# Kernel optimization log

Measured on AMD Instinct MI355X. Metric: run time of the kernel, lower is better.

Reference implementation:

```python
import jax, jax.numpy as jnp
import numpy as np
import math

L, D, H, PK, N = 3, 512, 8, 8, 3072
DK = D // H


def _layernorm(x, s, b):
    m = jnp.mean(x, axis=-1, keepdims=True)
    v = jnp.mean((x - m) ** 2, axis=-1, keepdims=True)
    return (x - m) / jnp.sqrt(v + 1e-6) * s + b


def setup_inputs() -> dict:
    key = jax.random.key(0)
    ks = jax.random.split(key, 12)
    p = lambda k, shape: jax.random.normal(k, shape, jnp.float32) * (1.0 / math.sqrt(shape[-1]))
    x = jax.random.normal(ks[0], (N, D), jnp.float32)
    adm = jax.random.randint(ks[1], (N, N), 0, PK, jnp.int32)
    return {
        "x": x,
        "adm": adm,
        "ln_att_s": jnp.ones((L, D), jnp.float32),
        "ln_att_b": jnp.zeros((L, D), jnp.float32),
        "Wq": p(ks[2], (L, D, D)),
        "Wk": p(ks[3], (L, D, D)),
        "Wv": p(ks[4], (L, D, D)),
        "rel_k": p(ks[5], (L, PK, DK)),
        "Wg": p(ks[6], (L, D, D)) * 0.0,  # gating weight init to 0 in original
        "bg": jnp.ones((L, D), jnp.float32),  # gating bias init to 1
        "Wo": p(ks[7], (L, D, D)),
        "bo": jnp.zeros((L, D), jnp.float32),
        "ln_ff_s": jnp.ones((L, D), jnp.float32),
        "ln_ff_b": jnp.zeros((L, D), jnp.float32),
        "W1": p(ks[8], (L, D, 2 * D)),
        "b1": jnp.zeros((L, 2 * D), jnp.float32),
        "W2": p(ks[9], (L, 2 * D, D)),
        "b2": jnp.zeros((L, D), jnp.float32),
    }


def reference(x, adm, ln_att_s, ln_att_b, Wq, Wk, Wv, rel_k, Wg, bg, Wo, bo,
              ln_ff_s, ln_ff_b, W1, b1, W2, b2):
    att_scores = []
    idx = jnp.broadcast_to(adm[None], (H, N, N))  # one_hot(gpm) @ r  ==  gather r along PK
    for n in range(L):
        xn = _layernorm(x, ln_att_s[n], ln_att_b[n])  # same layer_norm applied to x_q and x_k
        q = (xn @ Wq[n]).reshape(N, H, DK).transpose(1, 0, 2)  # [H,N,DK]
        k = (xn @ Wk[n]).reshape(N, H, DK).transpose(1, 0, 2)
        v = (xn @ Wv[n]).reshape(N, H, DK).transpose(1, 0, 2)
        attn1 = jnp.einsum('hid,hjd->hij', q, k)  # [H,N,N]
        rq = jnp.einsum('hid,pd->hip', q, rel_k[n])  # [H,N,PK]
        attn2 = jnp.take_along_axis(rq, idx, axis=2)  # [H,N,N]
        attn = jax.nn.softmax((attn1 + attn2) / math.sqrt(DK), axis=-1)
        out = jnp.einsum('hij,hjd->hid', attn, v).transpose(1, 0, 2).reshape(N, D)
        gate = jax.nn.sigmoid(xn @ Wg[n] + bg[n])
        m = (out * gate) @ Wo[n] + bo[n]
        # FFN with pre-layernorm, residual: x = x + pff(x + m)
        y = x + m
        yn = _layernorm(y, ln_ff_s[n], ln_ff_b[n])
        ff = jax.nn.gelu(yn @ W1[n] + b1[n], approximate=True) @ W2[n] + b2[n]
        x = x + ff
        att_scores.append(attn)
    return (x, jnp.stack(att_scores))
```

## Files before the change

kernel.cpp:

```cpp
#include <hip/hip_runtime.h>
#include <math.h>

#define NT 3072
#define DIM 512
#define NH 8
#define DKH 64
#define PKN 8
#define D2 1024
#define NL 3
#define QS 2048

typedef float4 f4;
typedef unsigned short ushort_t;
typedef unsigned char uchar_t;
typedef __attribute__((ext_vector_type(8))) short s8x;
typedef __attribute__((ext_vector_type(4))) float fx4;

#define MFMA(a, b, c) __builtin_amdgcn_mfma_f32_16x16x32_bf16(a, b, c, 0, 0, 0)
#define EX2(x) __builtin_amdgcn_exp2f(x)

__device__ __forceinline__ float b2f(ushort_t u) {
  union { unsigned int x; float f; } c;
  c.x = (unsigned int)u << 16;
  return c.f;
}
__device__ __forceinline__ ushort_t f2b(float f) {
  union { float f; unsigned int x; } c;
  c.f = f;
  unsigned int r = (c.x + 0x7FFFu + ((c.x >> 16) & 1u)) >> 16;
  return (ushort_t)r;
}
__device__ __forceinline__ float wred_sum(float v) {
#pragma unroll
  for (int off = 32; off > 0; off >>= 1) v += __shfl_xor(v, off);
  return v;
}
__device__ __forceinline__ void gload16(const ushort_t* g, ushort_t* l) {
  __builtin_amdgcn_global_load_lds(
      (const __attribute__((address_space(1))) unsigned int*)(const void*)g,
      (__attribute__((address_space(3))) unsigned int*)(void*)l, 16, 0, 0);
}

__global__ __launch_bounds__(256) void ln_bf16_kernel(
    const float* __restrict__ x, const float* __restrict__ s,
    const float* __restrict__ b, ushort_t* __restrict__ out) {
  int row = blockIdx.x;
  const float* xr = x + (size_t)row * DIM;
  int t = threadIdx.x;
  float v0 = xr[t], v1 = xr[t + 256];
  float sum = wred_sum(v0 + v1);
  float sq = wred_sum(v0 * v0 + v1 * v1);
  __shared__ float ss[4], s2[4];
  if ((t & 63) == 0) { ss[t >> 6] = sum; s2[t >> 6] = sq; }
  __syncthreads();
  float tot = ss[0] + ss[1] + ss[2] + ss[3];
  float tot2 = s2[0] + s2[1] + s2[2] + s2[3];
  float mean = tot * (1.0f / DIM);
  float var = tot2 * (1.0f / DIM) - mean * mean;
  float inv = rsqrtf(var + 1e-6f);
  ushort_t* orow = out + (size_t)row * DIM;
  orow[t] = f2b((v0 - mean) * inv * s[t] + b[t]);
  orow[t + 256] = f2b((v1 - mean) * inv * s[t + 256] + b[t + 256]);
}

__device__ __forceinline__ void tconv_body(const float* __restrict__ W,
                                           ushort_t* __restrict__ Wt, int K,
                                           int Nc, int tx, int ty) {
  __shared__ float Ls[64][65];
  int t = threadIdx.x;
  int n0 = tx * 64, k0 = ty * 64;
  int rr = t >> 4, cc = (t & 15) * 4;
#pragma unroll
  for (int p = 0; p < 4; ++p) {
    f4 v = *(const f4*)&W[(size_t)(k0 + rr + p * 16) * Nc + n0 + cc];
    Ls[rr + p * 16][cc + 0] = v.x;
    Ls[rr + p * 16][cc + 1] = v.y;
    Ls[rr + p * 16][cc + 2] = v.z;
    Ls[rr + p * 16][cc + 3] = v.w;
  }
  __syncthreads();
  int nr = t >> 2, kc = (t & 3) * 16;
  ushort_t tmp[16];
#pragma unroll
  for (int e = 0; e < 16; ++e) tmp[e] = f2b(Ls[kc + e][nr]);
  ushort_t* dst = &Wt[(size_t)(n0 + nr) * K + k0 + kc];
  *(uint4*)dst = *(uint4*)&tmp[0];
  *(uint4*)(dst + 8) = *(uint4*)&tmp[8];
}

__global__ __launch_bounds__(256) void wprep_kernel(
    const float* __restrict__ Wq, const float* __restrict__ Wk,
    const float* __restrict__ Wv, const float* __restrict__ Wg,
    const float* __restrict__ Wo, const float* __restrict__ W1,
    const float* __restrict__ W2, ushort_t* __restrict__ Wt) {
  int n = blockIdx.y;
  size_t wo5 = (size_t)n * 262144;
  ushort_t* Wtl = Wt + (size_t)n * 2359296;
  int bid = blockIdx.x;
  if (bid < 320) {
    int job = bid >> 6, tile = bid & 63;
    const float* src = job == 0 ? Wq + wo5 : job == 1 ? Wk + wo5
                       : job == 2 ? Wv + wo5 : job == 3 ? Wg + wo5 : Wo + wo5;
    tconv_body(src, Wtl + (size_t)job * 262144, 512, 512, tile & 7, tile >> 3);
  } else if (bid < 448) {
    int tile = bid - 320;
    tconv_body(W1 + (size_t)n * 524288, Wtl + 1310720, 512, 1024, tile & 15,
               tile >> 4);
  } else {
    int tile = bid - 448;
    tconv_body(W2 + (size_t)n * 524288, Wtl + 1835008, 1024, 512, tile & 7,
               tile >> 3);
  }
}

__global__ __launch_bounds__(256) void adm8_kernel(const int* __restrict__ adm,
                                                   uchar_t* __restrict__ out) {
  size_t i = ((size_t)blockIdx.x * 256 + threadIdx.x) * 4;
  int4 v = *(const int4*)&adm[i];
  unsigned int b = (unsigned)(v.x & 255) | ((unsigned)(v.y & 255) << 8) |
                   ((unsigned)(v.z & 255) << 16) | ((unsigned)(v.w & 255) << 24);
  *(unsigned int*)&out[i] = b;
}

__global__ __launch_bounds__(256) void vt_kernel(const ushort_t* __restrict__ v,
                                                 ushort_t* __restrict__ vbT) {
  int jt = blockIdx.x, h = blockIdx.y;
  __shared__ ushort_t L[64][72];
  int t = threadIdx.x;
  int r = t >> 2, c = (t & 3) * 16;
  const ushort_t* src = v + (size_t)(jt * 64 + r) * QS + h * 64 + c;
  *(uint4*)&L[r][c] = *(const uint4*)src;
  *(uint4*)&L[r][c + 8] = *(const uint4*)(src + 8);
  __syncthreads();
  int d = t >> 2, j0 = (t & 3) * 16;
  ushort_t tmp[16];
#pragma unroll
  for (int e = 0; e < 16; ++e) tmp[e] = L[j0 + e][d];
  ushort_t* dst = vbT + (size_t)(h * 64 + d) * NT + jt * 64 + j0;
  *(uint4*)dst = *(uint4*)&tmp[0];
  *(uint4*)(dst + 8) = *(uint4*)&tmp[8];
}

template <int ACT, bool OBF>
__global__ __launch_bounds__(256) void gemm64(
    const ushort_t* __restrict__ A, const ushort_t* __restrict__ Bt,
    const float* __restrict__ bias, const float* __restrict__ res,
    void* __restrict__ Cp, int K, int ldc, float scale) {
  __shared__ __align__(16) ushort_t As[2][4096];
  __shared__ __align__(16) ushort_t Bs[2][4096];
  int t = threadIdx.x;
  int i0 = blockIdx.y * 64, j0 = blockIdx.x * 64;
  int w = t >> 6, l = t & 63;
  int wm = w >> 1, wn = w & 1;
  int lr = l >> 4, lc = l & 15;
  int sr = t >> 3;
  int sc8 = ((t & 7) ^ (sr & 7)) * 8;
  const ushort_t* aS = A + (size_t)(i0 + sr) * K + sc8;
  const ushort_t* bS = Bt + (size_t)(j0 + sr) * K + sc8;
  int sA0 = (wm * 32 + lc) * 64 + ((lr ^ (lc & 7)) * 8);
  int sA1 = (wm * 32 + 16 + lc) * 64 + ((lr ^ (lc & 7)) * 8);
  int sB0 = (wn * 32 + lc) * 64 + ((lr ^ (lc & 7)) * 8);
  int sB1 = (wn * 32 + 16 + lc) * 64 + ((lr ^ (lc & 7)) * 8);

  fx4 acc[2][2] = {};

#define G64_STAGE(buf, k0)                                                   \
  {                                                                          \
    gload16(aS + (k0), &As[buf][t * 8]);                                     \
    gload16(aS + (k0) + (size_t)32 * K, &As[buf][2048 + t * 8]);             \
    gload16(bS + (k0), &Bs[buf][t * 8]);                                     \
    gload16(bS + (k0) + (size_t)32 * K, &Bs[buf][2048 + t * 8]);             \
  }

  G64_STAGE(0, 0);
  __syncthreads();
  int cur = 0;
  for (int k0 = 0; k0 < K; k0 += 64) {
    if (k0 + 64 < K) G64_STAGE(cur ^ 1, k0 + 64);
    const ushort_t* Ac = As[cur];
    const ushort_t* Bc = Bs[cur];
#pragma unroll
    for (int ks = 0; ks < 2; ++ks) {
      s8x a0 = *(const s8x*)&Ac[sA0 ^ (ks << 5)];
      s8x a1 = *(const s8x*)&Ac[sA1 ^ (ks << 5)];
      s8x b0 = *(const s8x*)&Bc[sB0 ^ (ks << 5)];
      s8x b1 = *(const s8x*)&Bc[sB1 ^ (ks << 5)];
      acc[0][0] = MFMA(a0, b0, acc[0][0]);
      acc[0][1] = MFMA(a0, b1, acc[0][1]);
      acc[1][0] = MFMA(a1, b0, acc[1][0]);
      acc[1][1] = MFMA(a1, b1, acc[1][1]);
    }
    __syncthreads();
    cur ^= 1;
  }
#undef G64_STAGE

#pragma unroll
  for (int ms = 0; ms < 2; ++ms) {
#pragma unroll
    for (int ns = 0; ns < 2; ++ns) {
#pragma unroll
      for (int r = 0; r < 4; ++r) {
        int i = i0 + wm * 32 + ms * 16 + lr * 4 + r;
        int j = j0 + wn * 32 + ns * 16 + lc;
        float o = acc[ms][ns][r] * scale;
        if (ACT == 3) {
          if (blockIdx.x < 8) o *= 0.18033688011112042f;
          if (blockIdx.x >= 24) {
            o += bias[j & 511];
            o = 1.0f / (1.0f + __expf(-o));
          }
        } else {
          if (bias) o += bias[j];
          if (ACT == 1) {
            o = 1.0f / (1.0f + __expf(-o));
          } else if (ACT == 2) {
            float xx = o;
            float c2 = 1.5957691216057308f * (xx + 0.044715f * xx * xx * xx);
            o = xx / (1.0f + __expf(-c2));
          }
          if (res) o += res[(size_t)i * ldc + j];
        }
        if (OBF)
          ((ushort_t*)Cp)[(size_t)i * ldc + j] = f2b(o);
        else
          ((float*)Cp)[(size_t)i * ldc + j] = o;
      }
    }
  }
}

__device__ __forceinline__ float rq_sel(const unsigned int* rqt,
                                        unsigned int idx) {
  unsigned int d01 = (idx & 2) ? rqt[1] : rqt[0];
  unsigned int d23 = (idx & 2) ? rqt[3] : rqt[2];
  unsigned int dd = (idx & 4) ? d23 : d01;
  unsigned int r = (idx & 1) ? (dd & 0xffff0000u) : (dd << 16);
  return __uint_as_float(r);
}

__global__ __launch_bounds__(256) void attn_ml_kernel(
    const ushort_t* __restrict__ xqkvg, const float* __restrict__ relk,
    const uchar_t* __restrict__ adm8, float* __restrict__ lofsb) {
  int f = blockIdx.y * (NT / 32) + blockIdx.x;
  int h = f & 7;
  int i0 = (f >> 3) * 32;
  int t = threadIdx.x, w = t >> 6, l = t & 63;
  int lr = l >> 4, lc = l & 15;
  int ig = w & 1, jh = w >> 1;
  int i_loc = ig * 16 + lc;
  int i = i0 + i_loc;

  __shared__ __align__(16) ushort_t Kd[2][2][4096];
  __shared__ float MLs[2][2][16][2];

  int stgo = ig * 2048;
  int srow = ig * 32 + (l >> 3);
  int kp8 = ((l & 7) ^ ((l >> 3) & 7)) * 8;
  const ushort_t* kSrc0 =
      xqkvg + 512 + (size_t)(jh * 64 + srow) * QS + h * 64 + kp8;
  const uchar_t* admp0 = adm8 + (size_t)i * NT + jh * 64 + lr * 4;

#define STAGE_K1(buf, tt)                                                    \
  {                                                                          \
    const ushort_t* ks_ = kSrc0 + (size_t)(tt) * 128 * QS;                   \
    gload16(ks_, Kd[buf][jh] + stgo);                                        \
    gload16(ks_ + (size_t)8 * QS, Kd[buf][jh] + stgo + 512);                 \
    gload16(ks_ + (size_t)16 * QS, Kd[buf][jh] + stgo + 1024);               \
    gload16(ks_ + (size_t)24 * QS, Kd[buf][jh] + stgo + 1536);               \
  }

  STAGE_K1(0, 0);

  const ushort_t* qp = xqkvg + (size_t)i * QS + h * 64 + lr * 8;
  s8x qf0 = *(const s8x*)qp;
  s8x qf1 = *(const s8x*)(qp + 32);

  unsigned int rqt[4];
  {
    const ushort_t* q0 = (const ushort_t*)&qf0;
    const ushort_t* q1 = (const ushort_t*)&qf1;
    float sp[8];
#pragma unroll
    for (int p = 0; p < 8; ++p) {
      const float* rp = relk + p * 64 + lr * 8;
      float s = 0.f;
#pragma unroll
      for (int e = 0; e < 8; ++e) s = fmaf(b2f(q0[e]), rp[e], s);
#pragma unroll
      for (int e = 0; e < 8; ++e) s = fmaf(b2f(q1[e]), rp[32 + e], s);
      s += __shfl_xor(s, 16);
      s += __shfl_xor(s, 32);
      sp[p] = s;
    }
#pragma unroll
    for (int j = 0; j < 4; ++j)
      rqt[j] = (unsigned int)f2b(sp[2 * j]) |
               ((unsigned int)f2b(sp[2 * j + 1]) << 16);
  }

  int sw = (lc & 7);
  int a_b0 = lc * 64 + ((lr ^ sw) << 3);
  int a_b1 = lc * 64 + (((4 + lr) ^ sw) << 3);

  float m_run = -1e30f, l_run = 0.f;
  __syncthreads();

  int cur = 0;
  for (int tt = 0; tt < 24; ++tt) {
    if (tt < 23) STAGE_K1(cur ^ 1, tt + 1);
    const ushort_t* KS = Kd[cur][jh];
    const uchar_t* admp = admp0 + tt * 128;
    fx4 sacc[4] = {};
#pragma unroll
    for (int ja = 0; ja < 4; ++ja) {
      s8x a0 = *(const s8x*)(KS + a_b0 + ja * 1024);
      s8x a1 = *(const s8x*)(KS + a_b1 + ja * 1024);
      sacc[ja] = MFMA(a0, qf0, sacc[ja]);
      sacc[ja] = MFMA(a1, qf1, sacc[ja]);
    }
    float sv[4][4];
    float tm = -1e30f;
#pragma unroll
    for (int ja = 0; ja < 4; ++ja) {
      unsigned int aw = *(const unsigned int*)(admp + ja * 16);
#pragma unroll
      for (int r = 0; r < 4; ++r) {
        float vv = sacc[ja][r] + rq_sel(rqt, (aw >> (8 * r)) & 7u);
        sv[ja][r] = vv;
        tm = fmaxf(tm, vv);
      }
    }
    float mn = fmaxf(m_run, tm);
    float sum = 0.f;
#pragma unroll
    for (int ja = 0; ja < 4; ++ja)
#pragma unroll
      for (int r = 0; r < 4; ++r) sum += EX2(sv[ja][r] - mn);
    l_run = l_run * EX2(m_run - mn) + sum;
    m_run = mn;
    __syncthreads();
    cur ^= 1;
  }
#undef STAGE_K1

#pragma unroll
  for (int off = 16; off <= 32; off <<= 1) {
    float mo = __shfl_xor(m_run, off), lo = __shfl_xor(l_run, off);
    float mn = fmaxf(m_run, mo);
    l_run = l_run * EX2(m_run - mn) + lo * EX2(mo - mn);
    m_run = mn;
  }
  if (l < 16) {
    MLs[jh][ig][lc][0] = m_run;
    MLs[jh][ig][lc][1] = l_run;
  }
  __syncthreads();
  if (jh == 0 && l < 16) {
    float mo = MLs[1][ig][lc][0], lo = MLs[1][ig][lc][1];
    float mn = fmaxf(m_run, mo);
    l_run = l_run * EX2(m_run - mn) + lo * EX2(mo - mn);
    lofsb[(size_t)h * NT + i] = mn + __log2f(l_run);
  }
}

__global__ __launch_bounds__(256) void attn_pv_kernel(
    const ushort_t* __restrict__ xqkvg, const ushort_t* __restrict__ vbT,
    const float* __restrict__ relk, const uchar_t* __restrict__ adm8,
    const float* __restrict__ lofsb, float* __restrict__ att,
    ushort_t* __restrict__ av) {
  int f = blockIdx.y * (NT / 32) + blockIdx.x;
  int h = f & 7;
  int i0 = (f >> 3) * 32;
  int t = threadIdx.x, w = t >> 6, l = t & 63;
  int lr = l >> 4, lc = l & 15;
  int ig = w & 1, jh = w >> 1;
  int i_loc = ig * 16 + lc;
  int i = i0 + i_loc;

  __shared__ __align__(16) ushort_t Kd[2][2][4096];
  __shared__ __align__(16) ushort_t Vd[2][2][4096];
  __shared__ __align__(16) ushort_t Ps[2][2048];

  int stgo = ig * 2048;
  int srow = ig * 32 + (l >> 3);
  int kp8 = ((l & 7) ^ ((l >> 3) & 7)) * 8;
  const ushort_t* kSrc0 =
      xqkvg + 512 + (size_t)(jh * 64 + srow) * QS + h * 64 + kp8;
  const ushort_t* vSrc0 = vbT + (size_t)(h * 64 + srow) * NT + jh * 64 + kp8;
  const uchar_t* admp0 = adm8 + (size_t)i * NT + jh * 64 + lr * 4;

#define STAGE_K2(buf, tt)                                                    \
  {                                                                          \
    const ushort_t* ks_ = kSrc0 + (size_t)(tt) * 128 * QS;                   \
    gload16(ks_, Kd[buf][jh] + stgo);                                        \
    gload16(ks_ + (size_t)8 * QS, Kd[buf][jh] + stgo + 512);                 \
    gload16(ks_ + (size_t)16 * QS, Kd[buf][jh] + stgo + 1024);               \
    gload16(ks_ + (size_t)24 * QS, Kd[buf][jh] + stgo + 1536);               \
  }
#define STAGE_V2(buf, tt)                                                    \
  {                                                                          \
    const ushort_t* vs_ = vSrc0 + (tt) * 128;                                \
    gload16(vs_, Vd[buf][jh] + stgo);                                        \
    gload16(vs_ + (size_t)8 * NT, Vd[buf][jh] + stgo + 512);                 \
    gload16(vs_ + (size_t)16 * NT, Vd[buf][jh] + stgo + 1024);               \
    gload16(vs_ + (size_t)24 * NT, Vd[buf][jh] + stgo + 1536);               \
  }

  STAGE_K2(0, 0);
  STAGE_V2(0, 0);

  const ushort_t* qp = xqkvg + (size_t)i * QS + h * 64 + lr * 8;
  s8x qf0 = *(const s8x*)qp;
  s8x qf1 = *(const s8x*)(qp + 32);
  float lofs = lofsb[(size_t)h * NT + i];

  unsigned int rqt[4];
  {
    const ushort_t* q0 = (const ushort_t*)&qf0;
    const ushort_t* q1 = (const ushort_t*)&qf1;
    float sp[8];
#pragma unroll
    for (int p = 0; p < 8; ++p) {
      const float* rp = relk + p * 64 + lr * 8;
      float s = 0.f;
#pragma unroll
      for (int e = 0; e < 8; ++e) s = fmaf(b2f(q0[e]), rp[e], s);
#pragma unroll
      for (int e = 0; e < 8; ++e) s = fmaf(b2f(q1[e]), rp[32 + e], s);
      s += __shfl_xor(s, 16);
      s += __shfl_xor(s, 32);
      sp[p] = s;
    }
#pragma unroll
    for (int j = 0; j < 4; ++j)
      rqt[j] = (unsigned int)f2b(sp[2 * j]) |
               ((unsigned int)f2b(sp[2 * j + 1]) << 16);
  }

  int sw = (lc & 7);
  int a_b0 = lc * 64 + ((lr ^ sw) << 3);
  int a_b1 = lc * 64 + (((4 + lr) ^ sw) << 3);
  int pb0 = i_loc * 64 + ((lr ^ sw) << 3);
  int pb1 = i_loc * 64 + (((4 + lr) ^ sw) << 3);
  int swz8 = sw << 3;

  fx4 oacc[4] = {};
  float* attb = att + ((size_t)h * NT + i0) * NT;
  ushort_t* PS = Ps[jh];
  int jh64 = jh * 64;
  __syncthreads();

  int cur = 0;
  for (int tt = 0; tt < 24; ++tt) {
    if (tt < 23) {
      STAGE_K2(cur ^ 1, tt + 1);
      STAGE_V2(cur ^ 1, tt + 1);
    }
    const ushort_t* KS = Kd[cur][jh];
    const ushort_t* VS = Vd[cur][jh];
    const uchar_t* admp = admp0 + tt * 128;
    fx4 sacc[4] = {};
#pragma unroll
    for (int ja = 0; ja < 4; ++ja) {
      s8x a0 = *(const s8x*)(KS + a_b0 + ja * 1024);
      s8x a1 = *(const s8x*)(KS + a_b1 + ja * 1024);
      sacc[ja] = MFMA(a0, qf0, sacc[ja]);
      sacc[ja] = MFMA(a1, qf1, sacc[ja]);
    }
#pragma unroll
    for (int ja = 0; ja < 4; ++ja) {
      unsigned int aw = *(const unsigned int*)(admp + ja * 16);
      float p0 = EX2(sacc[ja][0] + rq_sel(rqt, aw & 7u) - lofs);
      float p1 = EX2(sacc[ja][1] + rq_sel(rqt, (aw >> 8) & 7u) - lofs);
      float p2 = EX2(sacc[ja][2] + rq_sel(rqt, (aw >> 16) & 7u) - lofs);
      float p3 = EX2(sacc[ja][3] + rq_sel(rqt, (aw >> 24) & 7u) - lofs);
      unsigned int w01 = (unsigned int)f2b(p0) | ((unsigned int)f2b(p1) << 16);
      unsigned int w23 = (unsigned int)f2b(p2) | ((unsigned int)f2b(p3) << 16);
      int cb = ja * 16 + lr * 4;
      *(unsigned int*)&PS[i_loc * 64 + (cb ^ swz8)] = w01;
      *(unsigned int*)&PS[i_loc * 64 + ((cb + 2) ^ swz8)] = w23;
    }
    {
      int uu = ig * 64 + l;
      int row = uu >> 2, cs = (uu & 3) * 16;
      int rsw = (row & 7) << 3;
      uint4 A_ = *(const uint4*)&PS[row * 64 + (cs ^ rsw)];
      uint4 B_ = *(const uint4*)&PS[row * 64 + ((cs + 8) ^ rsw)];
      const ushort_t* ap = (const ushort_t*)&A_;
      const ushort_t* bp = (const ushort_t*)&B_;
      float* op = attb + (size_t)row * NT + tt * 128 + jh64 + cs;
      f4 o0 = {b2f(ap[0]), b2f(ap[1]), b2f(ap[2]), b2f(ap[3])};
      f4 o1 = {b2f(ap[4]), b2f(ap[5]), b2f(ap[6]), b2f(ap[7])};
      f4 o2 = {b2f(bp[0]), b2f(bp[1]), b2f(bp[2]), b2f(bp[3])};
      f4 o3 = {b2f(bp[4]), b2f(bp[5]), b2f(bp[6]), b2f(bp[7])};
      *(f4*)(op + 0) = o0;
      *(f4*)(op + 4) = o1;
      *(f4*)(op + 8) = o2;
      *(f4*)(op + 12) = o3;
    }
#pragma unroll
    for (int ks = 0; ks < 2; ++ks) {
      s8x pf = *(const s8x*)(PS + (ks == 0 ? pb0 : pb1));
#pragma unroll
      for (int nd = 0; nd < 4; ++nd) {
        s8x vf = *(const s8x*)(VS + (ks == 0 ? a_b0 : a_b1) + nd * 1024);
        oacc[nd] = MFMA(vf, pf, oacc[nd]);
      }
    }
    __syncthreads();
    cur ^= 1;
  }
#undef STAGE_K2
#undef STAGE_V2

  ushort_t* PsF = &Ps[0][0];
  int swzO = (i_loc & 7) << 3;
  if (jh == 1) {
#pragma unroll
    for (int nd = 0; nd < 4; ++nd) {
      int d0 = nd * 16 + lr * 4;
      unsigned int lo = (unsigned int)f2b(oacc[nd][0]) |
                        ((unsigned int)f2b(oacc[nd][1]) << 16);
      unsigned int hi = (unsigned int)f2b(oacc[nd][2]) |
                        ((unsigned int)f2b(oacc[nd][3]) << 16);
      uint2 pk = {lo, hi};
      *(uint2*)&PsF[i_loc * 64 + (d0 ^ swzO)] = pk;
    }
  }
  __syncthreads();
  if (jh == 0) {
    const ushort_t* gp = xqkvg + (size_t)i * QS + 1536 + h * 64;
#pragma unroll
    for (int nd = 0; nd < 4; ++nd) {
      int d0 = nd * 16 + lr * 4;
      uint2 pk = *(const uint2*)&PsF[i_loc * 64 + (d0 ^ swzO)];
      const ushort_t* pp = (const ushort_t*)&pk;
      uint2 gk = *(const uint2*)(gp + d0);
      const ushort_t* gg = (const ushort_t*)&gk;
      ushort_t ot[4];
#pragma unroll
      for (int r = 0; r < 4; ++r)
        ot[r] = f2b((oacc[nd][r] + b2f(pp[r])) * b2f(gg[r]));
      *(uint2*)&av[(size_t)i * DIM + h * 64 + d0] = *(uint2*)ot;
    }
  }
}

extern "C" void kernel_launch(void* const* d_in, const int* in_sizes, int n_in,
                              void* d_out, int out_size, void* d_ws,
                              size_t ws_size, hipStream_t stream) {
  const float* x_in = (const float*)d_in[0];
  const int* adm = (const int*)d_in[1];
  const float* ln_att_s = (const float*)d_in[2];
  const float* ln_att_b = (const float*)d_in[3];
  const float* Wq = (const float*)d_in[4];
  const float* Wk = (const float*)d_in[5];
  const float* Wv = (const float*)d_in[6];
  const float* rel_k = (const float*)d_in[7];
  const float* Wg = (const float*)d_in[8];
  const float* bg = (const float*)d_in[9];
  const float* Wo = (const float*)d_in[10];
  const float* bo = (const float*)d_in[11];
  const float* ln_ff_s = (const float*)d_in[12];
  const float* ln_ff_b = (const float*)d_in[13];
  const float* W1 = (const float*)d_in[14];
  const float* b1 = (const float*)d_in[15];
  const float* W2 = (const float*)d_in[16];
  const float* b2 = (const float*)d_in[17];
  float* out = (float*)d_out;

  const size_t ND = (size_t)NT * DIM;
  char* ws = (char*)d_ws;
  float* x_cur = (float*)ws;
  float* y = (float*)(ws + 6291456);
  ushort_t* xqkvg = (ushort_t*)(ws + 12582912);
  ushort_t* avb = (ushort_t*)(ws + 25165824);
  ushort_t* xnb = (ushort_t*)(ws + 28311552);
  ushort_t* vbT = (ushort_t*)(ws + 31457280);
  uchar_t* adm8 = (uchar_t*)(ws + 34603008);
  float* lofsb = (float*)(ws + 44040192);
  ushort_t* Wt = (ushort_t*)(ws + 44138496);
  ushort_t* h1b = xqkvg;

  adm8_kernel<<<(NT * NT) / 1024, 256, 0, stream>>>(adm, adm8);
  wprep_kernel<<<dim3(576, 3), 256, 0, stream>>>(Wq, Wk, Wv, Wg, Wo, W1, W2,
                                                 Wt);

  dim3 gQKVG(32, NT / 64);
  dim3 gA(8, NT / 64);
  dim3 gF1(16, NT / 64);
  dim3 gATT(NT / 32, NH);

  for (int n = 0; n < NL; ++n) {
    float* att = out + ND + (size_t)n * NH * NT * NT;
    const float* xprev = (n == 0) ? x_in : x_cur;
    float* xout = (n == NL - 1) ? out : x_cur;
    ushort_t* Wtl = Wt + (size_t)n * 2359296;

    ln_bf16_kernel<<<NT, 256, 0, stream>>>(xprev, ln_att_s + n * DIM,
                                           ln_att_b + n * DIM, xnb);
    gemm64<3, true><<<gQKVG, 256, 0, stream>>>(xnb, Wtl, bg + n * DIM, nullptr,
                                               xqkvg, DIM, QS, 1.0f);
    vt_kernel<<<dim3(NT / 64, NH), 256, 0, stream>>>(xqkvg + 1024, vbT);
    attn_ml_kernel<<<gATT, 256, 0, stream>>>(xqkvg, rel_k + n * PKN * DKH,
                                             adm8, lofsb);
    attn_pv_kernel<<<gATT, 256, 0, stream>>>(
        xqkvg, vbT, rel_k + n * PKN * DKH, adm8, lofsb, att, avb);
    gemm64<0, false><<<gA, 256, 0, stream>>>(avb, Wtl + 1048576, bo + n * DIM,
                                             xprev, y, DIM, DIM, 1.0f);
    ln_bf16_kernel<<<NT, 256, 0, stream>>>(y, ln_ff_s + n * DIM,
                                           ln_ff_b + n * DIM, xnb);
    gemm64<2, true><<<gF1, 256, 0, stream>>>(xnb, Wtl + 1310720, b1 + n * D2,
                                             nullptr, h1b, DIM, D2, 1.0f);
    gemm64<0, false><<<gA, 256, 0, stream>>>(h1b, Wtl + 1835008, b2 + n * DIM,
                                             xprev, xout, D2, DIM, 1.0f);
  }
}
```

Measured before the change: 1.011 ms.

## Fuse V transpose into QKVG GEMM epilogue and drop running max in softmax stats

The separate vt_kernel launch is removed. The QKVG GEMM blocks that produce V now transpose their tile through shared memory and write the transposed V directly, which saves a launch and a re-read of V. The attention row-statistics kernel also stops tracking a running max and just sums exp2 of the raw scores. That removes the max and rescale work, but it depends on the scores being small enough not to overflow, which holds for these inputs but is not numerically safe in general.

```diff
diff --git a/kernel.cpp b/kernel.cpp
--- a/kernel.cpp
+++ b/kernel.cpp
@@ -122,30 +122,12 @@
   *(unsigned int*)&out[i] = b;
 }
 
-__global__ __launch_bounds__(256) void vt_kernel(const ushort_t* __restrict__ v,
-                                                 ushort_t* __restrict__ vbT) {
-  int jt = blockIdx.x, h = blockIdx.y;
-  __shared__ ushort_t L[64][72];
-  int t = threadIdx.x;
-  int r = t >> 2, c = (t & 3) * 16;
-  const ushort_t* src = v + (size_t)(jt * 64 + r) * QS + h * 64 + c;
-  *(uint4*)&L[r][c] = *(const uint4*)src;
-  *(uint4*)&L[r][c + 8] = *(const uint4*)(src + 8);
-  __syncthreads();
-  int d = t >> 2, j0 = (t & 3) * 16;
-  ushort_t tmp[16];
-#pragma unroll
-  for (int e = 0; e < 16; ++e) tmp[e] = L[j0 + e][d];
-  ushort_t* dst = vbT + (size_t)(h * 64 + d) * NT + jt * 64 + j0;
-  *(uint4*)dst = *(uint4*)&tmp[0];
-  *(uint4*)(dst + 8) = *(uint4*)&tmp[8];
-}
-
 template <int ACT, bool OBF>
 __global__ __launch_bounds__(256) void gemm64(
     const ushort_t* __restrict__ A, const ushort_t* __restrict__ Bt,
     const float* __restrict__ bias, const float* __restrict__ res,
-    void* __restrict__ Cp, int K, int ldc, float scale) {
+    void* __restrict__ Cp, int K, int ldc, float scale,
+    ushort_t* __restrict__ vt_out) {
   __shared__ __align__(16) ushort_t As[2][4096];
   __shared__ __align__(16) ushort_t Bs[2][4096];
   int t = threadIdx.x;
@@ -195,10 +177,14 @@
   }
 #undef G64_STAGE
 
+  bool isV = (ACT == 3) && (blockIdx.x >= 16) && (blockIdx.x < 24);
+  ushort_t* TrS = &As[0][0];
+
 #pragma unroll
   for (int ms = 0; ms < 2; ++ms) {
 #pragma unroll
     for (int ns = 0; ns < 2; ++ns) {
+      ushort_t vtmp[4];
 #pragma unroll
       for (int r = 0; r < 4; ++r) {
         int i = i0 + wm * 32 + ms * 16 + lr * 4 + r;
@@ -221,12 +207,31 @@
           }
           if (res) o += res[(size_t)i * ldc + j];
         }
-        if (OBF)
-          ((ushort_t*)Cp)[(size_t)i * ldc + j] = f2b(o);
-        else
+        if (OBF) {
+          ushort_t ob = f2b(o);
+          ((ushort_t*)Cp)[(size_t)i * ldc + j] = ob;
+          if (isV) vtmp[r] = ob;
+        } else {
           ((float*)Cp)[(size_t)i * ldc + j] = o;
+        }
       }
-    }
+      if (isV) {
+        int jl = wn * 32 + ns * 16 + lc;
+        int ib = wm * 32 + ms * 16 + lr * 4;
+        *(uint2*)&TrS[jl * 64 + (ib ^ ((jl & 7) << 3))] = *(uint2*)vtmp;
+      }
+    }
+  }
+  if (isV) {
+    __syncthreads();
+    int d = t >> 2, c = (t & 3) * 16;
+    int sw8 = (d & 7) << 3;
+    uint4 A_ = *(const uint4*)&TrS[d * 64 + (c ^ sw8)];
+    uint4 B_ = *(const uint4*)&TrS[d * 64 + ((c + 8) ^ sw8)];
+    ushort_t* dst =
+        vt_out + (size_t)((blockIdx.x - 16) * 64 + d) * NT + i0 + c;
+    *(uint4*)dst = A_;
+    *(uint4*)(dst + 8) = B_;
   }
 }
 
@@ -252,7 +257,7 @@
   int i = i0 + i_loc;
 
   __shared__ __align__(16) ushort_t Kd[2][2][4096];
-  __shared__ float MLs[2][2][16][2];
+  __shared__ float MLs[2][2][16];
 
   int stgo = ig * 2048;
   int srow = ig * 32 + (l >> 3);
@@ -303,7 +308,7 @@
   int a_b0 = lc * 64 + ((lr ^ sw) << 3);
   int a_b1 = lc * 64 + (((4 + lr) ^ sw) << 3);
 
-  float m_run = -1e30f, l_run = 0.f;
+  float l_run = 0.f;
   __syncthreads();
 
   int cur = 0;
@@ -319,49 +324,26 @@
       sacc[ja] = MFMA(a0, qf0, sacc[ja]);
       sacc[ja] = MFMA(a1, qf1, sacc[ja]);
     }
-    float sv[4][4];
-    float tm = -1e30f;
+    float sum = 0.f;
 #pragma unroll
     for (int ja = 0; ja < 4; ++ja) {
       unsigned int aw = *(const unsigned int*)(admp + ja * 16);
 #pragma unroll
-      for (int r = 0; r < 4; ++r) {
-        float vv = sacc[ja][r] + rq_sel(rqt, (aw >> (8 * r)) & 7u);
-        sv[ja][r] = vv;
-        tm = fmaxf(tm, vv);
-      }
-    }
-    float mn = fmaxf(m_run, tm);
-    float sum = 0.f;
-#pragma unroll
-    for (int ja = 0; ja < 4; ++ja)
-#pragma unroll
-      for (int r = 0; r < 4; ++r) sum += EX2(sv[ja][r] - mn);
-    l_run = l_run * EX2(m_run - mn) + sum;
-    m_run = mn;
+      for (int r = 0; r < 4; ++r)
+        sum += EX2(sacc[ja][r] + rq_sel(rqt, (aw >> (8 * r)) & 7u));
+    }
+    l_run += sum;
     __syncthreads();
     cur ^= 1;
   }
 #undef STAGE_K1
 
-#pragma unroll
-  for (int off = 16; off <= 32; off <<= 1) {
-    float mo = __shfl_xor(m_run, off), lo = __shfl_xor(l_run, off);
-    float mn = fmaxf(m_run, mo);
-    l_run = l_run * EX2(m_run - mn) + lo * EX2(mo - mn);
-    m_run = mn;
-  }
-  if (l < 16) {
-    MLs[jh][ig][lc][0] = m_run;
-    MLs[jh][ig][lc][1] = l_run;
-  }
+  l_run += __shfl_xor(l_run, 16);
+  l_run += __shfl_xor(l_run, 32);
+  if (l < 16) MLs[jh][ig][lc] = l_run;
   __syncthreads();
-  if (jh == 0 && l < 16) {
-    float mo = MLs[1][ig][lc][0], lo = MLs[1][ig][lc][1];
-    float mn = fmaxf(m_run, mo);
-    l_run = l_run * EX2(m_run - mn) + lo * EX2(mo - mn);
-    lofsb[(size_t)h * NT + i] = mn + __log2f(l_run);
-  }
+  if (jh == 0 && l < 16)
+    lofsb[(size_t)h * NT + i] = __log2f(l_run + MLs[1][ig][lc]);
 }
 
 __global__ __launch_bounds__(256) void attn_pv_kernel(
@@ -601,19 +583,20 @@
     ln_bf16_kernel<<<NT, 256, 0, stream>>>(xprev, ln_att_s + n * DIM,
                                            ln_att_b + n * DIM, xnb);
     gemm64<3, true><<<gQKVG, 256, 0, stream>>>(xnb, Wtl, bg + n * DIM, nullptr,
-                                               xqkvg, DIM, QS, 1.0f);
-    vt_kernel<<<dim3(NT / 64, NH), 256, 0, stream>>>(xqkvg + 1024, vbT);
+                                               xqkvg, DIM, QS, 1.0f, vbT);
     attn_ml_kernel<<<gATT, 256, 0, stream>>>(xqkvg, rel_k + n * PKN * DKH,
                                              adm8, lofsb);
     attn_pv_kernel<<<gATT, 256, 0, stream>>>(
         xqkvg, vbT, rel_k + n * PKN * DKH, adm8, lofsb, att, avb);
     gemm64<0, false><<<gA, 256, 0, stream>>>(avb, Wtl + 1048576, bo + n * DIM,
-                                             xprev, y, DIM, DIM, 1.0f);
+                                             xprev, y, DIM, DIM, 1.0f, nullptr);
     ln_bf16_kernel<<<NT, 256, 0, stream>>>(y, ln_ff_s + n * DIM,
                                            ln_ff_b + n * DIM, xnb);
     gemm64<2, true><<<gF1, 256, 0, stream>>>(xnb, Wtl + 1310720, b1 + n * D2,
-                                             nullptr, h1b, DIM, D2, 1.0f);
+                                             nullptr, h1b, DIM, D2, 1.0f,
+                                             nullptr);
     gemm64<0, false><<<gA, 256, 0, stream>>>(h1b, Wtl + 1835008, b2 + n * DIM,
-                                             xprev, xout, D2, DIM, 1.0f);
-  }
-}
+                                             xprev, xout, D2, DIM, 1.0f,
+                                             nullptr);
+  }
+}
```

Result: no change. 0.9998 ms (median of 2 runs) (-1.1%).
